# Kernel optimization log

Measured on AMD Instinct MI355X. Metric: run time of the kernel, lower is better.

## Reference

```python
import jax, jax.numpy as jnp
import numpy as np

T = 4            # number of node types (len(output_sizes))
N = 16384        # nodes per type
D_IN = 512       # input_size
D_H = 1024       # hidden_size
OUT_SIZES = (128, 96, 64, 32)
MAX_OUT = max(OUT_SIZES)


def setup_inputs() -> dict:
    key = jax.random.key(0)
    ks = jax.random.split(key, 16)
    inp = {}
    for t in range(T):
        inp[f"x{t}"] = jax.random.normal(ks[t], (N, D_IN), jnp.float32)
    # nodes are grouped by type (sorted), matching the padded dict layout
    inp["node_type"] = jnp.repeat(jnp.arange(T, dtype=jnp.int64), N)
    # layer1: per-type Linear(input_size, hidden_size) (apply_net)
    inp["W1"] = jax.random.normal(ks[4], (T, D_IN, D_H), jnp.float32) * 0.02
    inp["b1"] = jnp.zeros((T, D_H), jnp.float32)
    # layer2: per-type Linear(hidden_size, out_size_t)
    for t in range(T):
        inp[f"W2_{t}"] = jax.random.normal(ks[5 + t], (D_H, OUT_SIZES[t]), jnp.float32) * 0.02
        inp[f"b2_{t}"] = jnp.zeros((OUT_SIZES[t],), jnp.float32)
    return inp


def reference(x0, x1, x2, x3, node_type, W1, b1,
              W2_0, b2_0, W2_1, b2_1, W2_2, b2_2, W2_3, b2_3):
    # Per-type gather is implicit: x{t} already holds the features of the
    # nodes whose node_type == t (node_type is sorted/blocked).
    xs = jnp.stack([x0, x1, x2, x3])                       # [T, N, D_IN]
    # apply_net: layer1 per type + activation (batched grouped-GEMM)
    h = jax.nn.relu(jnp.einsum('tni,tih->tnh', xs, W1) + b1[:, None, :])  # [T, N, D_H]
    W2s = (W2_0, W2_1, W2_2, W2_3)
    b2s = (b2_0, b2_1, b2_2, b2_3)
    outs = []
    for t in range(T):  # fixed small set of structurally distinct heads
        o = h[t] @ W2s[t] + b2s[t]                         # [N, out_t]
        outs.append(jnp.pad(o, ((0, 0), (0, MAX_OUT - o.shape[1]))))  # _pad to MAX_OUT
    return jnp.stack(outs)                                 # [T, N, MAX_OUT]
```

## Files before the change

kernel.cpp:

```cpp
#include <hip/hip_runtime.h>
#include <hip/hip_bf16.h>


typedef __attribute__((ext_vector_type(8))) short short8;
typedef __attribute__((ext_vector_type(4))) float f32x4;

#define NT 4
#define NNODE 16384
#define DIN 512
#define DH 1024
#define MAXO 128

static __device__ __forceinline__ ushort f2bf(float f) {
    __hip_bfloat16 h = __float2bfloat16(f);
    return *reinterpret_cast<ushort*>(&h);
}

#define GLD(gsrc, ldst)                                                        \
    __builtin_amdgcn_global_load_lds(                                          \
        (const __attribute__((address_space(1))) void*)(gsrc),                 \
        (__attribute__((address_space(3))) void*)(ldst), 16, 0, 0)

__global__ __launch_bounds__(256) void cvt_x_kernel(
    const float* __restrict__ x0, const float* __restrict__ x1,
    const float* __restrict__ x2, const float* __restrict__ x3,
    ushort* __restrict__ out) {
    const int i = blockIdx.x * 256 + threadIdx.x;
    const int per_t = (NNODE * DIN) / 8;
    const int t = i >> 20;
    const int loc = i & (per_t - 1);
    const float* x = (t == 0) ? x0 : (t == 1) ? x1 : (t == 2) ? x2 : x3;
    const float4* xv = reinterpret_cast<const float4*>(x) + (size_t)loc * 2;
    float4 a = xv[0], b = xv[1];
    union { short8 v; ushort u[8]; } r;
    float f[8] = {a.x, a.y, a.z, a.w, b.x, b.y, b.z, b.w};
#pragma unroll
    for (int j = 0; j < 8; ++j) r.u[j] = f2bf(f[j]);
    reinterpret_cast<short8*>(out)[i] = r.v;
}

__global__ __launch_bounds__(256) void cvt_w_t_kernel(
    const float* __restrict__ in, ushort* __restrict__ out,
    int R, int Cin, size_t in_tstride, size_t out_tstride) {
    __shared__ float tile[32][33];
    const int t = blockIdx.z;
    in += (size_t)t * in_tstride;
    out += (size_t)t * out_tstride;
    const int c0 = blockIdx.x * 32, r0 = blockIdx.y * 32;
    const int cx = threadIdx.x & 31;
    const int ry = threadIdx.x >> 5;
#pragma unroll
    for (int j = 0; j < 4; ++j) {
        int rr = ry + j * 8;
        int c = c0 + cx;
        tile[rr][cx] = (c < Cin) ? in[(size_t)(r0 + rr) * Cin + c] : 0.0f;
    }
    __syncthreads();
#pragma unroll
    for (int j = 0; j < 4; ++j) {
        int cc = ry + j * 8;
        out[(size_t)(c0 + cc) * R + r0 + cx] = f2bf(tile[cx][cc]);
    }
}

__global__ void pad_b2_kernel(const float* __restrict__ b0, const float* __restrict__ b1,
                              const float* __restrict__ b2, const float* __restrict__ b3,
                              float* __restrict__ out) {
    const int i = threadIdx.x;
    const int t = i >> 7, n = i & 127;
    const int sz[4] = {128, 96, 64, 32};
    const float* b = (t == 0) ? b0 : (t == 1) ? b1 : (t == 2) ? b2 : b3;
    out[i] = (n < sz[t]) ? b[n] : 0.0f;
}

template <int BN, bool RELU, bool OUTBF16>
__global__ __launch_bounds__(512, 1) void gemm2p(
    const ushort* __restrict__ Abase, const ushort* __restrict__ Bbase,
    const float* __restrict__ biasbase, void* __restrict__ Cbase,
    int M, int N, int K, int MT,
    size_t strideA, size_t strideB, size_t strideBias, size_t strideC) {
    constexpr int NF = BN / 64;
    constexpr int NBU = BN / 128;
    constexpr int ABYTES = 256 * 64 * 2;
    constexpr int BBYTES = BN * 64 * 2;
    constexpr int BUFBYTES = ABYTES + BBYTES;
    __shared__ char lds[2 * BUFBYTES];

    const int cpx = gridDim.x >> 3;
    const int g = blockIdx.x;
    const int wg = (g & 7) * cpx + (g >> 3);
    const int NTL = N / BN;
    const int t = wg / (MT * NTL);
    const int rmn = wg % (MT * NTL);
    const int m0 = (rmn / NTL) * 256;
    const int n0 = (rmn % NTL) * BN;

    const ushort* A = Abase + (size_t)t * strideA;
    const ushort* Bp = Bbase + (size_t)t * strideB;
    const float* bias = biasbase + (size_t)t * strideBias;

    const int tid = threadIdx.x;
    const int lane = tid & 63;
    const int w = tid >> 6;
    const int wm = w >> 2, wn = w & 3;
    const int lrow = lane & 15, lgrp = lane >> 4;

    const ushort* asrc[2][2];
    const ushort* bsrc[NBU][2];
    int adst[2][2], bdst[NBU][2];
#pragma unroll
    for (int j = 0; j < 2; ++j) {
        const int cc = j * 512 + tid;
        const int lr = cc >> 3;
        const int cbs = ((cc & 7) * 16) ^ ((lr & 7) << 4);
#pragma unroll
        for (int u = 0; u < 2; ++u) {
            asrc[u][j] = A + (size_t)(m0 + (lr >> 6) * 128 + u * 64 + (lr & 63)) * K
                           + (cbs >> 1);
            adst[u][j] = u * 16384 + cc * 16;
        }
#pragma unroll
        for (int u = 0; u < NBU; ++u) {
            bsrc[u][j] = Bp + (size_t)(n0 + u * 128 + lr) * K + (cbs >> 1);
            bdst[u][j] = ABYTES + u * 16384 + cc * 16;
        }
    }

    f32x4 acc[8][NF] = {};
    const int NK = K / 64;

#pragma unroll
    for (int u = 0; u < NBU; ++u) {
        GLD(bsrc[u][0], lds + bdst[u][0]);
        GLD(bsrc[u][1], lds + bdst[u][1]);
    }
#pragma unroll
    for (int u = 0; u < 2; ++u) {
        GLD(asrc[u][0], lds + adst[u][0]);
        GLD(asrc[u][1], lds + adst[u][1]);
    }
    asm volatile("s_waitcnt vmcnt(0)" ::: "memory");
    __builtin_amdgcn_s_barrier();

    for (int i = 0; i < NK; ++i) {
        const int cur = i & 1;
        const int nxtoff = (cur ^ 1) * BUFBYTES;
        const int ktn = (i + 1) * 64;
        const bool st = (i + 1 < NK);
        const char* Al = lds + cur * BUFBYTES;
        const char* Bl = Al + ABYTES;
        short8 bfr[NF][2];

        {
#pragma unroll
            for (int kkk = 0; kkk < 2; ++kkk)
#pragma unroll
                for (int ni = 0; ni < NF; ++ni) {
                    const int br = wn * (NF * 16) + ni * 16 + lrow;
                    const int kb = (kkk * 64 + lgrp * 16) ^ ((br & 7) << 4);
                    bfr[ni][kkk] = *(const short8*)(Bl + br * 128 + kb);
                }
            short8 af[4][2];
#pragma unroll
            for (int kkk = 0; kkk < 2; ++kkk)
#pragma unroll
                for (int ml = 0; ml < 4; ++ml) {
                    const int lr = wm * 64 + ml * 16 + lrow;
                    const int kb = (kkk * 64 + lgrp * 16) ^ ((lr & 7) << 4);
                    af[ml][kkk] = *(const short8*)(Al + lr * 128 + kb);
                }
            if (st) {
#pragma unroll
                for (int u = 0; u < NBU; ++u) {
                    GLD(bsrc[u][0] + ktn, lds + nxtoff + bdst[u][0]);
                    GLD(bsrc[u][1] + ktn, lds + nxtoff + bdst[u][1]);
                }
            }
            asm volatile("" ::: "memory");
            __builtin_amdgcn_s_barrier();
            __builtin_amdgcn_sched_barrier(0);
            __builtin_amdgcn_s_setprio(1);
#pragma unroll
            for (int kkk = 0; kkk < 2; ++kkk)
#pragma unroll
                for (int ml = 0; ml < 4; ++ml)
#pragma unroll
                    for (int ni = 0; ni < NF; ++ni)
                        acc[ml][ni] = __builtin_amdgcn_mfma_f32_16x16x32_bf16(
                            bfr[ni][kkk], af[ml][kkk], acc[ml][ni], 0, 0, 0);
            __builtin_amdgcn_s_setprio(0);
            if (st) {
                if constexpr (NBU == 2)
                    asm volatile("s_waitcnt vmcnt(4)" ::: "memory");
                else
                    asm volatile("s_waitcnt vmcnt(2)" ::: "memory");
            } else {
                asm volatile("s_waitcnt vmcnt(0)" ::: "memory");
            }
            asm volatile("" ::: "memory");
            __builtin_amdgcn_s_barrier();
        }

        {
            short8 af[4][2];
#pragma unroll
            for (int kkk = 0; kkk < 2; ++kkk)
#pragma unroll
                for (int ml = 0; ml < 4; ++ml) {
                    const int lr = wm * 64 + ml * 16 + lrow;
                    const int kb = (kkk * 64 + lgrp * 16) ^ ((lr & 7) << 4);
                    af[ml][kkk] = *(const short8*)(Al + 16384 + lr * 128 + kb);
                }
            if (st) {
                GLD(asrc[0][0] + ktn, lds + nxtoff + adst[0][0]);
                GLD(asrc[0][1] + ktn, lds + nxtoff + adst[0][1]);
                GLD(asrc[1][0] + ktn, lds + nxtoff + adst[1][0]);
                GLD(asrc[1][1] + ktn, lds + nxtoff + adst[1][1]);
            }
            asm volatile("" ::: "memory");
            __builtin_amdgcn_s_barrier();
            __builtin_amdgcn_sched_barrier(0);
            __builtin_amdgcn_s_setprio(1);
#pragma unroll
            for (int kkk = 0; kkk < 2; ++kkk)
#pragma unroll
                for (int ml = 0; ml < 4; ++ml)
#pragma unroll
                    for (int ni = 0; ni < NF; ++ni)
                        acc[4 + ml][ni] = __builtin_amdgcn_mfma_f32_16x16x32_bf16(
                            bfr[ni][kkk], af[ml][kkk], acc[4 + ml][ni], 0, 0, 0);
            __builtin_amdgcn_s_setprio(0);
            if (st) asm volatile("s_waitcnt vmcnt(2)" ::: "memory");
            asm volatile("" ::: "memory");
            __builtin_amdgcn_s_barrier();
        }
    }

    const int wnoff = n0 + wn * (NF * 16);
    const int wmoff = m0 + wm * 128;
#pragma unroll
    for (int ni = 0; ni < NF; ++ni) {
        const int ncol = wnoff + ni * 16 + lgrp * 4;
        const float4 bv = *reinterpret_cast<const float4*>(&bias[ncol]);
#pragma unroll
        for (int mi = 0; mi < 8; ++mi) {
            const int row = wmoff + mi * 16 + lrow;
            float v0 = acc[mi][ni][0] + bv.x;
            float v1 = acc[mi][ni][1] + bv.y;
            float v2 = acc[mi][ni][2] + bv.z;
            float v3 = acc[mi][ni][3] + bv.w;
            if (RELU) {
                v0 = fmaxf(v0, 0.0f); v1 = fmaxf(v1, 0.0f);
                v2 = fmaxf(v2, 0.0f); v3 = fmaxf(v3, 0.0f);
            }
            const size_t base = (size_t)t * strideC + (size_t)row * N + ncol;
            if (OUTBF16) {
                uint2 p;
                p.x = (uint)f2bf(v0) | ((uint)f2bf(v1) << 16);
                p.y = (uint)f2bf(v2) | ((uint)f2bf(v3) << 16);
                *reinterpret_cast<uint2*>(&((ushort*)Cbase)[base]) = p;
            } else {
                float4 p = {v0, v1, v2, v3};
                *reinterpret_cast<float4*>(&((float*)Cbase)[base]) = p;
            }
        }
    }
}

extern "C" void kernel_launch(void* const* d_in, const int* in_sizes, int n_in,
                              void* d_out, int out_size, void* d_ws, size_t ws_size,
                              hipStream_t stream) {
    const float* x0 = (const float*)d_in[0];
    const float* x1 = (const float*)d_in[1];
    const float* x2 = (const float*)d_in[2];
    const float* x3 = (const float*)d_in[3];
    const float* W1 = (const float*)d_in[5];
    const float* b1 = (const float*)d_in[6];
    const float* W2[4] = {(const float*)d_in[7], (const float*)d_in[9],
                          (const float*)d_in[11], (const float*)d_in[13]};
    const float* b2[4] = {(const float*)d_in[8], (const float*)d_in[10],
                          (const float*)d_in[12], (const float*)d_in[14]};

    char* ws = (char*)d_ws;
    ushort* H   = (ushort*)ws;
    ushort* Xbf = (ushort*)(ws + 134217728ull);
    ushort* W1T = (ushort*)(ws + 134217728ull + 67108864ull);
    ushort* W2T = (ushort*)(ws + 134217728ull + 67108864ull + 4194304ull);
    float*  b2p = (float*)(ws + 134217728ull + 67108864ull + 4194304ull + 1048576ull);

    cvt_x_kernel<<<16384, 256, 0, stream>>>(x0, x1, x2, x3, Xbf);
    cvt_w_t_kernel<<<dim3(32, 16, 4), 256, 0, stream>>>(
        W1, W1T, DIN, DH, (size_t)DIN * DH, (size_t)DH * DIN);
    const int osz[4] = {128, 96, 64, 32};
    for (int t = 0; t < 4; ++t)
        cvt_w_t_kernel<<<dim3(4, 32, 1), 256, 0, stream>>>(
            W2[t], W2T + (size_t)t * MAXO * DH, DH, osz[t], 0, 0);
    pad_b2_kernel<<<1, 512, 0, stream>>>(b2[0], b2[1], b2[2], b2[3], b2p);

    gemm2p<256, true, true><<<1024, 512, 0, stream>>>(
        Xbf, W1T, b1, H,
        NNODE, DH, DIN, NNODE / 256,
        (size_t)NNODE * DIN, (size_t)DH * DIN, (size_t)DH, (size_t)NNODE * DH);

    gemm2p<128, false, false><<<256, 512, 0, stream>>>(
        H, W2T, b2p, d_out,
        NNODE, MAXO, DH, NNODE / 256,
        (size_t)NNODE * DH, (size_t)MAXO * DH, (size_t)MAXO, (size_t)NNODE * MAXO);
}
```

Baseline: 179.3 us.

## Replace split two-phase K-loop with single-barrier double-buffered pipeline

Replaces the GEMM main loop, which split each K-step into two half-M phases with interleaved partial prefetches and four barriers, with a simpler structure. All A and B tiles for the next K-step are issued up front, the full 8x NF MFMA block runs per k-substep, and the loop ends with one wait and one barrier. The goal is to cut barrier and waitcnt overhead and give each wave longer uninterrupted MFMA runs. The trade-offs are that every load is drained with vmcnt(0) each iteration, the finer load/compute interleaving is lost, and more A fragments are held live in registers at once.

```diff
diff --git a/kernel.cpp b/kernel.cpp
--- a/kernel.cpp
+++ b/kernel.cpp
@@ -74,17 +74,17 @@
 }
 
 template <int BN, bool RELU, bool OUTBF16>
-__global__ __launch_bounds__(512, 1) void gemm2p(
+__global__ __launch_bounds__(512, 1) void gemm1b(
     const ushort* __restrict__ Abase, const ushort* __restrict__ Bbase,
     const float* __restrict__ biasbase, void* __restrict__ Cbase,
-    int M, int N, int K, int MT,
+    int N, int K, int MT,
     size_t strideA, size_t strideB, size_t strideBias, size_t strideC) {
     constexpr int NF = BN / 64;
-    constexpr int NBU = BN / 128;
+    constexpr int NBC = BN * 8 / 512;
     constexpr int ABYTES = 256 * 64 * 2;
     constexpr int BBYTES = BN * 64 * 2;
-    constexpr int BUFBYTES = ABYTES + BBYTES;
-    __shared__ char lds[2 * BUFBYTES];
+    constexpr int BUF = ABYTES + BBYTES;
+    __shared__ char lds[2 * BUF];
 
     const int cpx = gridDim.x >> 3;
     const int g = blockIdx.x;
@@ -105,134 +105,80 @@
     const int wm = w >> 2, wn = w & 3;
     const int lrow = lane & 15, lgrp = lane >> 4;
 
-    const ushort* asrc[2][2];
-    const ushort* bsrc[NBU][2];
-    int adst[2][2], bdst[NBU][2];
-#pragma unroll
-    for (int j = 0; j < 2; ++j) {
-        const int cc = j * 512 + tid;
-        const int lr = cc >> 3;
-        const int cbs = ((cc & 7) * 16) ^ ((lr & 7) << 4);
-#pragma unroll
-        for (int u = 0; u < 2; ++u) {
-            asrc[u][j] = A + (size_t)(m0 + (lr >> 6) * 128 + u * 64 + (lr & 63)) * K
-                           + (cbs >> 1);
-            adst[u][j] = u * 16384 + cc * 16;
-        }
-#pragma unroll
-        for (int u = 0; u < NBU; ++u) {
-            bsrc[u][j] = Bp + (size_t)(n0 + u * 128 + lr) * K + (cbs >> 1);
-            bdst[u][j] = ABYTES + u * 16384 + cc * 16;
-        }
+    const ushort* asrc[4];
+    int adst[4];
+#pragma unroll
+    for (int j = 0; j < 4; ++j) {
+        const int c = j * 512 + tid;
+        const int r = c >> 3;
+        const int cb = ((c & 7) * 16) ^ ((r & 7) << 4);
+        asrc[j] = A + (size_t)(m0 + r) * K + (cb >> 1);
+        adst[j] = c * 16;
+    }
+    const ushort* bsrc[NBC];
+    int bdst[NBC];
+#pragma unroll
+    for (int j = 0; j < NBC; ++j) {
+        const int c = j * 512 + tid;
+        const int r = c >> 3;
+        const int cb = ((c & 7) * 16) ^ ((r & 7) << 4);
+        bsrc[j] = Bp + (size_t)(n0 + r) * K + (cb >> 1);
+        bdst[j] = ABYTES + c * 16;
     }
 
     f32x4 acc[8][NF] = {};
     const int NK = K / 64;
 
 #pragma unroll
-    for (int u = 0; u < NBU; ++u) {
-        GLD(bsrc[u][0], lds + bdst[u][0]);
-        GLD(bsrc[u][1], lds + bdst[u][1]);
-    }
-#pragma unroll
-    for (int u = 0; u < 2; ++u) {
-        GLD(asrc[u][0], lds + adst[u][0]);
-        GLD(asrc[u][1], lds + adst[u][1]);
-    }
+    for (int j = 0; j < 4; ++j) GLD(asrc[j], lds + adst[j]);
+#pragma unroll
+    for (int j = 0; j < NBC; ++j) GLD(bsrc[j], lds + bdst[j]);
     asm volatile("s_waitcnt vmcnt(0)" ::: "memory");
     __builtin_amdgcn_s_barrier();
+    __builtin_amdgcn_sched_barrier(0);
 
     for (int i = 0; i < NK; ++i) {
-        const int cur = i & 1;
-        const int nxtoff = (cur ^ 1) * BUFBYTES;
+        const char* cu_ = lds + (i & 1) * BUF;
+        char* nx_ = lds + ((i + 1) & 1) * BUF;
         const int ktn = (i + 1) * 64;
         const bool st = (i + 1 < NK);
-        const char* Al = lds + cur * BUFBYTES;
-        const char* Bl = Al + ABYTES;
-        short8 bfr[NF][2];
-
-        {
-#pragma unroll
-            for (int kkk = 0; kkk < 2; ++kkk)
-#pragma unroll
-                for (int ni = 0; ni < NF; ++ni) {
-                    const int br = wn * (NF * 16) + ni * 16 + lrow;
-                    const int kb = (kkk * 64 + lgrp * 16) ^ ((br & 7) << 4);
-                    bfr[ni][kkk] = *(const short8*)(Bl + br * 128 + kb);
-                }
-            short8 af[4][2];
-#pragma unroll
-            for (int kkk = 0; kkk < 2; ++kkk)
-#pragma unroll
-                for (int ml = 0; ml < 4; ++ml) {
-                    const int lr = wm * 64 + ml * 16 + lrow;
-                    const int kb = (kkk * 64 + lgrp * 16) ^ ((lr & 7) << 4);
-                    af[ml][kkk] = *(const short8*)(Al + lr * 128 + kb);
-                }
-            if (st) {
-#pragma unroll
-                for (int u = 0; u < NBU; ++u) {
-                    GLD(bsrc[u][0] + ktn, lds + nxtoff + bdst[u][0]);
-                    GLD(bsrc[u][1] + ktn, lds + nxtoff + bdst[u][1]);
-                }
-            }
-            asm volatile("" ::: "memory");
+
+        if (st) {
+#pragma unroll
+            for (int j = 0; j < 4; ++j) GLD(asrc[j] + ktn, nx_ + adst[j]);
+#pragma unroll
+            for (int j = 0; j < NBC; ++j) GLD(bsrc[j] + ktn, nx_ + bdst[j]);
+        }
+
+#pragma unroll
+        for (int kkk = 0; kkk < 2; ++kkk) {
+            short8 bfr[NF], af[8];
+#pragma unroll
+            for (int ni = 0; ni < NF; ++ni) {
+                const int br = wn * (NF * 16) + ni * 16 + lrow;
+                const int kb = (kkk * 64 + lgrp * 16) ^ ((br & 7) << 4);
+                bfr[ni] = *(const short8*)(cu_ + ABYTES + br * 128 + kb);
+            }
+#pragma unroll
+            for (int ml = 0; ml < 8; ++ml) {
+                const int ar = wm * 128 + ml * 16 + lrow;
+                const int kb = (kkk * 64 + lgrp * 16) ^ ((ar & 7) << 4);
+                af[ml] = *(const short8*)(cu_ + ar * 128 + kb);
+            }
+            __builtin_amdgcn_s_setprio(1);
+#pragma unroll
+            for (int ml = 0; ml < 8; ++ml)
+#pragma unroll
+                for (int ni = 0; ni < NF; ++ni)
+                    acc[ml][ni] = __builtin_amdgcn_mfma_f32_16x16x32_bf16(
+                        bfr[ni], af[ml], acc[ml][ni], 0, 0, 0);
+            __builtin_amdgcn_s_setprio(0);
+        }
+
+        if (st) {
+            asm volatile("s_waitcnt vmcnt(0)" ::: "memory");
             __builtin_amdgcn_s_barrier();
             __builtin_amdgcn_sched_barrier(0);
-            __builtin_amdgcn_s_setprio(1);
-#pragma unroll
-            for (int kkk = 0; kkk < 2; ++kkk)
-#pragma unroll
-                for (int ml = 0; ml < 4; ++ml)
-#pragma unroll
-                    for (int ni = 0; ni < NF; ++ni)
-                        acc[ml][ni] = __builtin_amdgcn_mfma_f32_16x16x32_bf16(
-                            bfr[ni][kkk], af[ml][kkk], acc[ml][ni], 0, 0, 0);
-            __builtin_amdgcn_s_setprio(0);
-            if (st) {
-                if constexpr (NBU == 2)
-                    asm volatile("s_waitcnt vmcnt(4)" ::: "memory");
-                else
-                    asm volatile("s_waitcnt vmcnt(2)" ::: "memory");
-            } else {
-                asm volatile("s_waitcnt vmcnt(0)" ::: "memory");
-            }
-            asm volatile("" ::: "memory");
-            __builtin_amdgcn_s_barrier();
-        }
-
-        {
-            short8 af[4][2];
-#pragma unroll
-            for (int kkk = 0; kkk < 2; ++kkk)
-#pragma unroll
-                for (int ml = 0; ml < 4; ++ml) {
-                    const int lr = wm * 64 + ml * 16 + lrow;
-                    const int kb = (kkk * 64 + lgrp * 16) ^ ((lr & 7) << 4);
-                    af[ml][kkk] = *(const short8*)(Al + 16384 + lr * 128 + kb);
-                }
-            if (st) {
-                GLD(asrc[0][0] + ktn, lds + nxtoff + adst[0][0]);
-                GLD(asrc[0][1] + ktn, lds + nxtoff + adst[0][1]);
-                GLD(asrc[1][0] + ktn, lds + nxtoff + adst[1][0]);
-                GLD(asrc[1][1] + ktn, lds + nxtoff + adst[1][1]);
-            }
-            asm volatile("" ::: "memory");
-            __builtin_amdgcn_s_barrier();
-            __builtin_amdgcn_sched_barrier(0);
-            __builtin_amdgcn_s_setprio(1);
-#pragma unroll
-            for (int kkk = 0; kkk < 2; ++kkk)
-#pragma unroll
-                for (int ml = 0; ml < 4; ++ml)
-#pragma unroll
-                    for (int ni = 0; ni < NF; ++ni)
-                        acc[4 + ml][ni] = __builtin_amdgcn_mfma_f32_16x16x32_bf16(
-                            bfr[ni][kkk], af[ml][kkk], acc[4 + ml][ni], 0, 0, 0);
-            __builtin_amdgcn_s_setprio(0);
-            if (st) asm volatile("s_waitcnt vmcnt(2)" ::: "memory");
-            asm volatile("" ::: "memory");
-            __builtin_amdgcn_s_barrier();
         }
     }
 
@@ -297,13 +243,13 @@
             W2[t], W2T + (size_t)t * MAXO * DH, DH, osz[t], 0, 0);
     pad_b2_kernel<<<1, 512, 0, stream>>>(b2[0], b2[1], b2[2], b2[3], b2p);
 
-    gemm2p<256, true, true><<<1024, 512, 0, stream>>>(
+    gemm1b<256, true, true><<<1024, 512, 0, stream>>>(
         Xbf, W1T, b1, H,
-        NNODE, DH, DIN, NNODE / 256,
+        DH, DIN, NNODE / 256,
         (size_t)NNODE * DIN, (size_t)DH * DIN, (size_t)DH, (size_t)NNODE * DH);
 
-    gemm2p<128, false, false><<<256, 512, 0, stream>>>(
+    gemm1b<128, false, false><<<256, 512, 0, stream>>>(
         H, W2T, b2p, d_out,
-        NNODE, MAXO, DH, NNODE / 256,
+        MAXO, DH, NNODE / 256,
         (size_t)NNODE * DH, (size_t)MAXO * DH, (size_t)MAXO, (size_t)NNODE * MAXO);
 }
```

After: 178.4 us. No clear change (-0.5%).
